# Performance work log

Hardware: AMD Instinct MI355X
Metric: run time of the kernel (lower is better)

The kernel has to match this reference:

```python
import jax, jax.numpy as jnp
import numpy as np
from jax import lax

E = 5          # experts
CIN = 256      # in_planes
COUT = 256     # out_planes
K = 3          # kernel_size
HID = CIN // 4 + 1  # attention hidden dim
STRIDE = 1
PAD = 1


def setup_inputs() -> dict:
    key = jax.random.key(0)
    k_x, k_w, k_a1, k_a2 = jax.random.split(key, 4)
    B, H, W = 32, 56, 56
    x = jax.random.normal(k_x, (B, CIN, H, W), dtype=jnp.float32)
    # expert conv weights (E, O, I, K, K), kaiming-uniform-ish scale
    fan_in = CIN * K * K
    bound = float(np.sqrt(6.0 / fan_in))
    weight = jax.random.uniform(k_w, (E, COUT, CIN, K, K), dtype=jnp.float32,
                                minval=-bound, maxval=bound)
    # align_conv initialized as per-expert identity mixing matrix (E, O, O)
    align_mat = jnp.tile(jnp.eye(COUT, dtype=jnp.float32)[None], (E, 1, 1))
    # attention MLP (1x1 convs on pooled features == matmuls)
    att_w1 = jax.random.normal(k_a1, (HID, CIN), dtype=jnp.float32) * float(np.sqrt(2.0 / CIN))
    att_w2 = jax.random.normal(k_a2, (E, HID), dtype=jnp.float32) * float(np.sqrt(2.0 / HID))
    att_b2 = jnp.zeros((E,), dtype=jnp.float32)
    return {"x": x, "weight": weight, "align_mat": align_mat,
            "att_w1": att_w1, "att_w2": att_w2, "att_b2": att_b2}


def _ada_agg_forward(x, weight, align_mat, att_w1, att_w2, att_b2):
    # attention: global avg pool -> 1x1 conv -> relu -> 1x1 conv -> sigmoid
    s = jnp.mean(x, axis=(2, 3))                      # (B, CIN)
    h = jax.nn.relu(jnp.einsum('bc,hc->bh', s, att_w1))  # (B, HID)
    attn = jax.nn.sigmoid(jnp.einsum('bh,eh->be', h, att_w2) + att_b2)  # (B, E)

    # align: per-expert channel remix of expert weights
    # W'_e[j] = sum_o align_mat[e, j, o] * W_e[o]
    w_aligned = jnp.einsum('ejo,eoixy->ejixy', align_mat, weight)  # (E, O, I, K, K)

    # per-sample aggregated weights
    agg_w = jnp.einsum('be,eoixy->boixy', attn, w_aligned)  # (B, O, I, K, K)

    # per-sample conv (the torch groups=batch trick), vectorized with vmap
    def conv_one(xi, wi):
        # xi: (CIN, H, W), wi: (O, I, K, K)
        return lax.conv_general_dilated(
            xi[None], wi,
            window_strides=(STRIDE, STRIDE),
            padding=((PAD, PAD), (PAD, PAD)),
            dimension_numbers=('NCHW', 'OIHW', 'NCHW'))[0]

    return jax.vmap(conv_one)(x, agg_w)  # (B, O, H', W')


def reference(x, weight, align_mat, att_w1, att_w2, att_b2):
    return _ada_agg_forward(x, weight, align_mat, att_w1, att_w2, att_b2)
```

## Files before the change

kernel.cpp:

```cpp
#include <hip/hip_runtime.h>
#include <hip/hip_bf16.h>

#define BATCH 32
#define CIN   256
#define COUT  256
#define HH    56
#define HP    58
#define NEXP  5
#define HID   65

#define OFF_S     0
#define OFF_ATTN  32768
#define OFF_WAL   65536
#define OFF_AGGW  (12u*1024u*1024u)
#define OFF_XPAD  (48u*1024u*1024u)

typedef __bf16 bf16x8 __attribute__((ext_vector_type(8)));
typedef float  f32x4  __attribute__((ext_vector_type(4)));

__device__ __forceinline__ unsigned short f2bf(float f) {
    unsigned int u = __float_as_uint(f);
    unsigned int r = (u + 0x7FFFu + ((u >> 16) & 1u)) >> 16;
    return (unsigned short)r;
}

#define AS1 __attribute__((address_space(1)))
#define AS3 __attribute__((address_space(3)))
__device__ __forceinline__ void gl_lds16(const unsigned short* g, unsigned short* l) {
    __builtin_amdgcn_global_load_lds((const AS1 void*)g, (AS3 void*)l, 16, 0, 0);
}

#define XLP 132
__global__ void xprep_kernel(const float* __restrict__ x,
                             unsigned short* __restrict__ xpad,
                             float* __restrict__ s) {
    const int y0 = blockIdx.x * 2, c0 = blockIdx.y * 128, b = blockIdx.z;
    const int tid = threadIdx.x, lane = tid & 63, wg = tid >> 6;
    __shared__ unsigned short lds[2 * HH * XLP];

    {
        const uint4 z = make_uint4(0, 0, 0, 0);
        if (blockIdx.x == 0) {
            uint4* p = (uint4*)(xpad + (size_t)(b * HP * HP) * 256 + c0);
            for (int i = tid; i < HP * 16; i += 256)
                p[(i >> 4) * 32 + (i & 15)] = z;
        }
        if (blockIdx.x == 27) {
            uint4* p = (uint4*)(xpad + (size_t)((b * HP + 57) * HP) * 256 + c0);
            for (int i = tid; i < HP * 16; i += 256)
                p[(i >> 4) * 32 + (i & 15)] = z;
        }
        if (tid < 64) {
            const int r = y0 + 1 + (tid >> 5);
            const int cc = ((tid >> 4) & 1) * 57;
            uint4* p = (uint4*)(xpad + (size_t)((b * HP + r) * HP + cc) * 256 + c0);
            p[tid & 15] = z;
        }
    }

    #pragma unroll 2
    for (int cc = wg; cc < 128; cc += 4) {
        if (lane < HH) {
            const float2 v = *(const float2*)&x[
                (size_t)((b * 256 + c0 + cc) * HH + y0) * HH + lane * 2];
            const int p = lane * 2;
            const int r0 = p / HH, x0 = p - r0 * HH;
            const int q = p + 1;
            const int r1 = q / HH, x1 = q - r1 * HH;
            lds[(r0 * HH + x0) * XLP + cc] = f2bf(v.x);
            lds[(r1 * HH + x1) * XLP + cc] = f2bf(v.y);
        }
    }
    __syncthreads();
    {
        const int r = tid >> 7, c = tid & 127;
        float sum = 0.f;
        for (int xx = 0; xx < HH; ++xx) {
            const unsigned int u = lds[(r * HH + xx) * XLP + c];
            sum += __uint_as_float(u << 16);
        }
        atomicAdd(&s[b * 256 + c0 + c], sum);
    }
    for (int i = tid; i < 2 * HH * 32; i += 256) {
        const int r = (i >= HH * 32) ? 1 : 0;
        const int rem = i - r * HH * 32;
        const int xx = rem >> 5, cq = (rem & 31) * 4;
        const uint2 v = *(const uint2*)&lds[(r * HH + xx) * XLP + cq];
        *(uint2*)(xpad + (size_t)(((b * HP + y0 + r + 1) * HP + (xx + 1))) * 256
                  + c0 + cq) = v;
    }
}

__global__ void attn_kernel(const float* __restrict__ s,
                            const float* __restrict__ w1,
                            const float* __restrict__ w2,
                            const float* __restrict__ b2,
                            float* __restrict__ attn) {
    const int b = blockIdx.x, tid = threadIdx.x;
    __shared__ float sm[256];
    __shared__ float part[130];
    __shared__ float hm[HID];
    sm[tid] = s[b * 256 + tid] * (1.f / 3136.f);
    __syncthreads();
    if (tid < 130) {
        const int h = (tid >= 65) ? tid - 65 : tid;
        const int base = (tid >= 65) ? 128 : 0;
        float acc = 0.f;
        #pragma unroll 4
        for (int c = 0; c < 128; ++c) acc += sm[base + c] * w1[h * 256 + base + c];
        part[tid] = acc;
    }
    __syncthreads();
    if (tid < HID) hm[tid] = fmaxf(part[tid] + part[tid + 65], 0.f);
    __syncthreads();
    if (tid < NEXP) {
        float acc = b2[tid];
        for (int j = 0; j < HID; ++j) acc += hm[j] * w2[tid * HID + j];
        attn[b * NEXP + tid] = 1.f / (1.f + expf(-acc));
    }
}

__global__ void align_kernel(const float* __restrict__ am,
                             const float* __restrict__ w,
                             float* __restrict__ wal) {
    const int nt = blockIdx.x, jt = blockIdx.y, e = blockIdx.z;
    const int tid = threadIdx.x;
    const int tj = tid >> 5, tn = tid & 31;
    __shared__ float At[64][33];
    __shared__ float Wt[32][128];
    float acc[8][4];
    #pragma unroll
    for (int a = 0; a < 8; ++a)
        #pragma unroll
        for (int c = 0; c < 4; ++c) acc[a][c] = 0.f;

    for (int o0 = 0; o0 < 256; o0 += 32) {
        {
            const int row = tid >> 2, col = (tid & 3) * 8;
            const float* src = am + (size_t)((e * 256) + jt * 64 + row) * 256 + o0 + col;
            float4 v0 = *(const float4*)(src);
            float4 v1 = *(const float4*)(src + 4);
            *(float4*)&At[row][col] = v0;
            *(float4*)&At[row][col + 4] = v1;
        }
        {
            const int row = tid >> 3, col = (tid & 7) * 16;
            const float* src = w + (size_t)((e * 256) + o0 + row) * 2304 + nt * 128 + col;
            #pragma unroll
            for (int q = 0; q < 4; ++q)
                *(float4*)&Wt[row][col + q * 4] = *(const float4*)(src + q * 4);
        }
        __syncthreads();
        for (int k = 0; k < 32; ++k) {
            float wv[4];
            #pragma unroll
            for (int c = 0; c < 4; ++c) wv[c] = Wt[k][tn * 4 + c];
            #pragma unroll
            for (int a = 0; a < 8; ++a) {
                const float av = At[tj * 8 + a][k];
                #pragma unroll
                for (int c = 0; c < 4; ++c) acc[a][c] += av * wv[c];
            }
        }
        __syncthreads();
    }
    #pragma unroll
    for (int a = 0; a < 8; ++a) {
        const int j = jt * 64 + tj * 8 + a;
        #pragma unroll
        for (int c = 0; c < 4; ++c) {
            const int n = nt * 128 + tn * 4 + c;
            const int t = n % 9, i = n / 9;
            wal[(size_t)(((e * 9 + t) * 256 + j)) * 256 + i] = acc[a][c];
        }
    }
}

__global__ void agg_kernel(const float* __restrict__ wal,
                           const float* __restrict__ attn,
                           unsigned short* __restrict__ aggw) {
    const int t = blockIdx.x >> 6;
    const int j = (blockIdx.x & 63) * 4 + (threadIdx.x >> 6);
    const int i = (threadIdx.x & 63) * 4;
    __shared__ float at[BATCH * NEXP];
    if (threadIdx.x < BATCH * NEXP) at[threadIdx.x] = attn[threadIdx.x];
    float4 wv[NEXP];
    #pragma unroll
    for (int e = 0; e < NEXP; ++e)
        wv[e] = *(const float4*)&wal[(size_t)(((e * 9 + t) * 256 + j)) * 256 + i];
    __syncthreads();
    for (int b = 0; b < BATCH; ++b) {
        float4 acc = make_float4(0.f, 0.f, 0.f, 0.f);
        #pragma unroll
        for (int e = 0; e < NEXP; ++e) {
            const float a = at[b * NEXP + e];
            acc.x += a * wv[e].x; acc.y += a * wv[e].y;
            acc.z += a * wv[e].z; acc.w += a * wv[e].w;
        }
        uint2 pk;
        pk.x = (unsigned)f2bf(acc.x) | ((unsigned)f2bf(acc.y) << 16);
        pk.y = (unsigned)f2bf(acc.z) | ((unsigned)f2bf(acc.w) << 16);
        *(uint2*)&aggw[(size_t)(((b * 9 + t) * 256 + j)) * 256 + i] = pk;
    }
}

__global__ __launch_bounds__(256, 3) void conv_kernel(
        const unsigned short* __restrict__ xpad,
        const unsigned short* __restrict__ aggw,
        float* __restrict__ out) {
    const int blk = blockIdx.x;
    const int xcd = blk & 7, slot = blk >> 3;
    const int b = xcd * 4 + slot / 49;
    const int pos = slot % 49;
    const int y0 = (pos / 7) * 8, x0 = (pos % 7) * 8;
    const int tid = threadIdx.x;
    const int wm = tid >> 6, lane = tid & 63;
    const int quad = lane >> 4, ln = lane & 15;

    __shared__ unsigned short ldsA[2 * 8192];
    __shared__ unsigned short ldsB[2 * 3200];

    f32x4 acc[4][4];
    #pragma unroll
    for (int mt = 0; mt < 4; ++mt)
        #pragma unroll
        for (int nt = 0; nt < 4; ++nt) acc[mt][nt] = (f32x4){0.f, 0.f, 0.f, 0.f};

    int nb[4];
    #pragma unroll
    for (int nt = 0; nt < 4; ++nt)
        nb[nt] = ((((ln >> 3) + nt * 2) * 40 + (ln & 7) * 4 + quad)) * 16;

    const int abase = wm * 4096 + (ln * 4 + quad) * 16;

    const unsigned short* aspb;
    int aldsu[4];
    {
        aspb = aggw + (size_t)(b * 9) * 65536;
        #pragma unroll
        for (int k = 0; k < 4; ++k) aldsu[k] = (tid + k * 256) * 8;
    }
    int asrc[4];
    #pragma unroll
    for (int k = 0; k < 4; ++k) {
        const int u = tid + k * 256;
        asrc[k] = (u >> 2) * 256 + (u & 3) * 8;
    }

    const unsigned short* bsp[2];
    int bldsu[2];
    #pragma unroll
    for (int k = 0; k < 2; ++k) {
        int u = tid + k * 256; if (u > 399) u = 399;
        const int r = u / 40, rem = u - r * 40;
        const int c = rem >> 2, sub = rem & 3;
        bsp[k] = xpad + (size_t)(((b * HP + y0 + r) * HP + x0 + c)) * 256 + sub * 8;
        bldsu[k] = u * 8;
    }

    #pragma unroll
    for (int k = 0; k < 4; ++k) gl_lds16(aspb + asrc[k], ldsA + aldsu[k]);
    gl_lds16(bsp[0], ldsB + bldsu[0]);
    if (tid < 144) gl_lds16(bsp[1], ldsB + bldsu[1]);
    __syncthreads();

    int pa = 0, pb = 0;
    #pragma unroll 1
    for (int c0 = 0; c0 < 256; c0 += 32) {
        #pragma unroll
        for (int tap = 0; tap < 9; ++tap) {
            if (!(c0 == 224 && tap == 8)) {
                const int ntap = (tap == 8) ? 0 : tap + 1;
                const int nc0 = (tap == 8) ? c0 + 32 : c0;
                const unsigned short* srcA = aspb + ntap * 65536 + nc0;
                unsigned short* dA = ldsA + (pa ^ 1) * 8192;
                #pragma unroll
                for (int k = 0; k < 4; ++k) gl_lds16(srcA + asrc[k], dA + aldsu[k]);
            }
            if (tap == 4 && c0 < 224) {
                unsigned short* dB = ldsB + (pb ^ 1) * 3200;
                gl_lds16(bsp[0] + c0 + 32, dB + bldsu[0]);
                if (tid < 144) gl_lds16(bsp[1] + c0 + 32, dB + bldsu[1]);
            }
            const int ky = tap / 3, kx = tap % 3;
            const char* lA = (const char*)ldsA + pa * 16384;
            const char* lB = (const char*)ldsB + pb * 6400;
            bf16x8 a[4];
            #pragma unroll
            for (int mt = 0; mt < 4; ++mt)
                a[mt] = *(const bf16x8*)(lA + mt * 1024 + abase);
            #pragma unroll
            for (int nt = 0; nt < 4; ++nt) {
                const bf16x8 bf = *(const bf16x8*)(lB +
                    nb[nt] + (ky * 40 + kx * 4) * 16);
                #pragma unroll
                for (int mt = 0; mt < 4; ++mt)
                    acc[mt][nt] = __builtin_amdgcn_mfma_f32_16x16x32_bf16(
                        a[mt], bf, acc[mt][nt], 0, 0, 0);
            }
            __syncthreads();
            pa ^= 1;
        }
        pb ^= 1;
    }

    #pragma unroll
    for (int mt = 0; mt < 4; ++mt) {
        #pragma unroll
        for (int nt = 0; nt < 4; ++nt) {
            const int yy = y0 + (ln >> 3) + nt * 2;
            const int xx = x0 + (ln & 7);
            #pragma unroll
            for (int r = 0; r < 4; ++r) {
                const int cout = wm * 64 + mt * 16 + quad * 4 + r;
                out[(size_t)(((b * 256 + cout) * HH + yy)) * HH + xx] = acc[mt][nt][r];
            }
        }
    }
}

extern "C" void kernel_launch(void* const* d_in, const int* in_sizes, int n_in,
                              void* d_out, int out_size, void* d_ws, size_t ws_size,
                              hipStream_t stream) {
    const float* x      = (const float*)d_in[0];
    const float* weight = (const float*)d_in[1];
    const float* am     = (const float*)d_in[2];
    const float* w1     = (const float*)d_in[3];
    const float* w2     = (const float*)d_in[4];
    const float* b2     = (const float*)d_in[5];
    float* out = (float*)d_out;
    char* ws = (char*)d_ws;

    float* s             = (float*)(ws + OFF_S);
    float* attn          = (float*)(ws + OFF_ATTN);
    float* wal           = (float*)(ws + OFF_WAL);
    unsigned short* aggw = (unsigned short*)(ws + OFF_AGGW);
    unsigned short* xpad = (unsigned short*)(ws + OFF_XPAD);

    hipMemsetAsync(s, 0, BATCH * 256 * sizeof(float), stream);
    xprep_kernel<<<dim3(28, 2, BATCH), 256, 0, stream>>>(x, xpad, s);
    attn_kernel<<<BATCH, 256, 0, stream>>>(s, w1, w2, b2, attn);
    align_kernel<<<dim3(18, 4, NEXP), 256, 0, stream>>>(am, weight, wal);
    agg_kernel<<<576, 256, 0, stream>>>(wal, attn, aggw);
    conv_kernel<<<1568, 256, 0, stream>>>(xpad, aggw, out);
}
```

Baseline: 434.9 us.

## Retile conv into 128-channel by 28x8-pixel blocks with wider per-wave N

The conv kernel now tiles each block as 128 output channels by a 28x8 spatial region instead of 256 channels by 8x8. Each wave covers 64 channels and 14x8 pixels with a 4x7 MFMA accumulator grid. The aim is higher arithmetic intensity per LDS load and less redundant halo loading of the input. The cost is more accumulator registers (occupancy bound lowered from 3 to 2 blocks) and only 896 blocks, which may fill the CUs less evenly.

Result: faster. 387.4 us (-10.9%).

```diff
diff --git a/kernel.cpp b/kernel.cpp
--- a/kernel.cpp
+++ b/kernel.cpp
@@ -204,64 +204,64 @@
     }
 }
 
-__global__ __launch_bounds__(256, 3) void conv_kernel(
+__global__ __launch_bounds__(256, 2) void conv_kernel(
         const unsigned short* __restrict__ xpad,
         const unsigned short* __restrict__ aggw,
         float* __restrict__ out) {
     const int blk = blockIdx.x;
     const int xcd = blk & 7, slot = blk >> 3;
-    const int b = xcd * 4 + slot / 49;
-    const int pos = slot % 49;
-    const int y0 = (pos / 7) * 8, x0 = (pos % 7) * 8;
+    const int b = xcd * 4 + slot / 28;
+    const int rem = slot % 28;
+    const int ch = rem & 1;
+    const int pos = rem >> 1;
+    const int x0 = (pos >> 1) * 8;
+    const int y0 = (pos & 1) * 28;
     const int tid = threadIdx.x;
-    const int wm = tid >> 6, lane = tid & 63;
+    const int w = tid >> 6, lane = tid & 63;
+    const int wm = w & 1, wp = w >> 1;
     const int quad = lane >> 4, ln = lane & 15;
 
-    __shared__ unsigned short ldsA[2 * 8192];
-    __shared__ unsigned short ldsB[2 * 3200];
-
-    f32x4 acc[4][4];
+    __shared__ unsigned short ldsA[2 * 4096];
+    __shared__ unsigned short ldsB[2 * 9600];
+
+    f32x4 acc[4][7];
     #pragma unroll
     for (int mt = 0; mt < 4; ++mt)
         #pragma unroll
-        for (int nt = 0; nt < 4; ++nt) acc[mt][nt] = (f32x4){0.f, 0.f, 0.f, 0.f};
-
-    int nb[4];
-    #pragma unroll
-    for (int nt = 0; nt < 4; ++nt)
-        nb[nt] = ((((ln >> 3) + nt * 2) * 40 + (ln & 7) * 4 + quad)) * 16;
+        for (int nt = 0; nt < 7; ++nt) acc[mt][nt] = (f32x4){0.f, 0.f, 0.f, 0.f};
+
+    int nb[7];
+    #pragma unroll
+    for (int nt = 0; nt < 7; ++nt)
+        nb[nt] = (((wp * 14 + (ln >> 3) + nt * 2) * 40 + (ln & 7) * 4 + quad)) * 16;
 
     const int abase = wm * 4096 + (ln * 4 + quad) * 16;
 
-    const unsigned short* aspb;
-    int aldsu[4];
-    {
-        aspb = aggw + (size_t)(b * 9) * 65536;
-        #pragma unroll
-        for (int k = 0; k < 4; ++k) aldsu[k] = (tid + k * 256) * 8;
-    }
-    int asrc[4];
-    #pragma unroll
-    for (int k = 0; k < 4; ++k) {
+    const unsigned short* aspb = aggw + (size_t)(b * 9) * 65536 + ch * 32768;
+    int aldsu[2], asrc[2];
+    #pragma unroll
+    for (int k = 0; k < 2; ++k) {
         const int u = tid + k * 256;
+        aldsu[k] = u * 8;
         asrc[k] = (u >> 2) * 256 + (u & 3) * 8;
     }
 
-    const unsigned short* bsp[2];
-    int bldsu[2];
-    #pragma unroll
-    for (int k = 0; k < 2; ++k) {
-        int u = tid + k * 256; if (u > 399) u = 399;
-        const int r = u / 40, rem = u - r * 40;
-        const int c = rem >> 2, sub = rem & 3;
+    const unsigned short* bsp[5];
+    int bldsu[5];
+    #pragma unroll
+    for (int k = 0; k < 5; ++k) {
+        int u = tid + k * 256; if (u > 1199) u = 1199;
+        const int r = u / 40, rm = u - r * 40;
+        const int c = rm >> 2, sub = rm & 3;
         bsp[k] = xpad + (size_t)(((b * HP + y0 + r) * HP + x0 + c)) * 256 + sub * 8;
         bldsu[k] = u * 8;
     }
 
     #pragma unroll
-    for (int k = 0; k < 4; ++k) gl_lds16(aspb + asrc[k], ldsA + aldsu[k]);
-    gl_lds16(bsp[0], ldsB + bldsu[0]);
-    if (tid < 144) gl_lds16(bsp[1], ldsB + bldsu[1]);
+    for (int k = 0; k < 2; ++k) gl_lds16(aspb + asrc[k], ldsA + aldsu[k]);
+    #pragma unroll
+    for (int k = 0; k < 4; ++k) gl_lds16(bsp[k], ldsB + bldsu[k]);
+    if (tid < 176) gl_lds16(bsp[4], ldsB + bldsu[4]);
     __syncthreads();
 
     int pa = 0, pb = 0;
@@ -273,24 +273,26 @@
                 const int ntap = (tap == 8) ? 0 : tap + 1;
                 const int nc0 = (tap == 8) ? c0 + 32 : c0;
                 const unsigned short* srcA = aspb + ntap * 65536 + nc0;
-                unsigned short* dA = ldsA + (pa ^ 1) * 8192;
+                unsigned short* dA = ldsA + (pa ^ 1) * 4096;
                 #pragma unroll
-                for (int k = 0; k < 4; ++k) gl_lds16(srcA + asrc[k], dA + aldsu[k]);
+                for (int k = 0; k < 2; ++k) gl_lds16(srcA + asrc[k], dA + aldsu[k]);
             }
             if (tap == 4 && c0 < 224) {
-                unsigned short* dB = ldsB + (pb ^ 1) * 3200;
-                gl_lds16(bsp[0] + c0 + 32, dB + bldsu[0]);
-                if (tid < 144) gl_lds16(bsp[1] + c0 + 32, dB + bldsu[1]);
+                unsigned short* dB = ldsB + (pb ^ 1) * 9600;
+                #pragma unroll
+                for (int k = 0; k < 4; ++k)
+                    gl_lds16(bsp[k] + c0 + 32, dB + bldsu[k]);
+                if (tid < 176) gl_lds16(bsp[4] + c0 + 32, dB + bldsu[4]);
             }
             const int ky = tap / 3, kx = tap % 3;
-            const char* lA = (const char*)ldsA + pa * 16384;
-            const char* lB = (const char*)ldsB + pb * 6400;
+            const char* lA = (const char*)ldsA + pa * 8192;
+            const char* lB = (const char*)ldsB + pb * 19200;
             bf16x8 a[4];
             #pragma unroll
             for (int mt = 0; mt < 4; ++mt)
                 a[mt] = *(const bf16x8*)(lA + mt * 1024 + abase);
             #pragma unroll
-            for (int nt = 0; nt < 4; ++nt) {
+            for (int nt = 0; nt < 7; ++nt) {
                 const bf16x8 bf = *(const bf16x8*)(lB +
                     nb[nt] + (ky * 40 + kx * 4) * 16);
                 #pragma unroll
@@ -307,12 +309,12 @@
     #pragma unroll
     for (int mt = 0; mt < 4; ++mt) {
         #pragma unroll
-        for (int nt = 0; nt < 4; ++nt) {
-            const int yy = y0 + (ln >> 3) + nt * 2;
+        for (int nt = 0; nt < 7; ++nt) {
+            const int yy = y0 + wp * 14 + (ln >> 3) + nt * 2;
             const int xx = x0 + (ln & 7);
             #pragma unroll
             for (int r = 0; r < 4; ++r) {
-                const int cout = wm * 64 + mt * 16 + quad * 4 + r;
+                const int cout = ch * 128 + wm * 64 + mt * 16 + quad * 4 + r;
                 out[(size_t)(((b * 256 + cout) * HH + yy)) * HH + xx] = acc[mt][nt][r];
             }
         }
@@ -342,5 +344,5 @@
     attn_kernel<<<BATCH, 256, 0, stream>>>(s, w1, w2, b2, attn);
     align_kernel<<<dim3(18, 4, NEXP), 256, 0, stream>>>(am, weight, wal);
     agg_kernel<<<576, 256, 0, stream>>>(wal, attn, aggw);
-    conv_kernel<<<1568, 256, 0, stream>>>(xpad, aggw, out);
-}
+    conv_kernel<<<896, 256, 0, stream>>>(xpad, aggw, out);
+}
```
